# Kernel tuning notes

Measured on AMD Instinct MI355X. Metric: run time of the kernel, lower is better.

The kernel has to match this reference:

```python
import jax, jax.numpy as jnp
import numpy as np

H = 2048      # hidden_size
F = 768       # moe_intermediate_size
E = 32        # num_experts
K = 4         # num_experts_per_tok (top_k)
SF = 5632     # shared_expert_intermediate_size
B, S = 1, 2048


def setup_inputs() -> dict:
    key = jax.random.key(0)
    ks = jax.random.split(key, 9)
    rn = lambda k, sh, sc: (jax.random.normal(k, sh, jnp.float32) * sc)
    return {
        "hidden_states": rn(ks[0], (B, S, H), 1.0),
        "gate_w": rn(ks[1], (H, E), 0.02),                 # router Linear(H->E), no bias
        "wg": rn(ks[2], (E, H, F), H ** -0.5),             # expert gate_proj
        "wu": rn(ks[3], (E, H, F), H ** -0.5),             # expert up_proj
        "wd": rn(ks[4], (E, F, H), F ** -0.5),             # expert down_proj
        "sg": rn(ks[5], (H, SF), H ** -0.5),               # shared expert gate_proj
        "su": rn(ks[6], (H, SF), H ** -0.5),               # shared expert up_proj
        "sd": rn(ks[7], (SF, H), SF ** -0.5),              # shared expert down_proj
        "seg": rn(ks[8], (H, 1), H ** -0.5),               # shared_expert_gate Linear(H->1)
    }


def _moe_forward(x, gate_w, wg, wu, wd, sg, su, sd, seg):
    # x: [T, H] flattened tokens
    T = x.shape[0]
    logits = x @ gate_w                                    # [T, E]
    probs = jax.nn.softmax(logits, axis=-1)
    topw, topi = jax.lax.top_k(probs, K)                   # [T, K]
    topw = topw / jnp.sum(topw, axis=-1, keepdims=True)    # norm_topk_prob=True
    # dense combine weights [T, E] (expert ids per token are unique -> set is safe)
    combine = jnp.zeros((T, E), x.dtype).at[jnp.arange(T)[:, None], topi].set(topw)

    def body(acc, ew):
        wg_e, wu_e, wd_e, c_e = ew                         # [H,F],[H,F],[F,H],[T]
        h = jax.nn.silu(x @ wg_e) * (x @ wu_e)             # [T, F]
        return acc + c_e[:, None] * (h @ wd_e), None

    out, _ = jax.lax.scan(body, jnp.zeros_like(x), (wg, wu, wd, combine.T))

    shared = (jax.nn.silu(x @ sg) * (x @ su)) @ sd         # [T, H]
    out = out + jax.nn.sigmoid(x @ seg) * shared
    return out


def reference(hidden_states, gate_w, wg, wu, wd, sg, su, sd, seg):
    b, s, h = hidden_states.shape
    x = hidden_states.reshape(-1, h)
    out = _moe_forward(x, gate_w, wg, wu, wd, sg, su, sd, seg)
    return out.reshape(b, s, h)
```

## Files before the change

kernel.cpp:

```cpp
#include <hip/hip_runtime.h>
#include <hip/hip_bf16.h>
#include <math.h>

#define H_DIM 2048
#define F_DIM 768
#define E_NUM 32
#define TOPK 4
#define SF_DIM 5632
#define T_NUM 2048
#define P_MAX (T_NUM * TOPK)

typedef __attribute__((ext_vector_type(8))) short short8v;
typedef __attribute__((ext_vector_type(4))) float f4;
typedef unsigned short u16;

__device__ __forceinline__ u16 f2b(float f) {
  unsigned int u = __float_as_uint(f);
  u += 0x7FFFu + ((u >> 16) & 1u);
  return (u16)(u >> 16);
}

__device__ __forceinline__ f4 mfma16(short8v a, short8v b, f4 c) {
  return __builtin_amdgcn_mfma_f32_16x16x32_bf16(a, b, c, 0, 0, 0);
}

__device__ __forceinline__ void gld16(const u16* g, u16* l) {
  __builtin_amdgcn_global_load_lds(
      (const __attribute__((address_space(1))) void*)g,
      (__attribute__((address_space(3))) void*)l, 16, 0, 0);
}

__global__ __launch_bounds__(64) void router_kernel(
    const float* __restrict__ x, const float* __restrict__ gate_w,
    const float* __restrict__ seg, int* __restrict__ cnt,
    int* __restrict__ toklist, int* __restrict__ slotE,
    int* __restrict__ slotPos, float* __restrict__ wt4,
    float* __restrict__ sigbuf) {
  const int t = blockIdx.x;
  const int l = threadIdx.x;
  const int e = l & 31;
  const int half = l >> 5;
  const float* xr = x + (size_t)t * H_DIM;

  float acc = 0.0f, aseg = 0.0f;
  const int h0 = half * (H_DIM / 2);
  for (int h = 0; h < H_DIM / 2; ++h) {
    float xv = xr[h0 + h];
    acc += xv * gate_w[(h0 + h) * E_NUM + e];
    aseg += xv * seg[h0 + h];
  }
  acc += __shfl_xor(acc, 32, 64);
  aseg += __shfl_xor(aseg, 32, 64);

  float m = acc;
#pragma unroll
  for (int mask = 16; mask >= 1; mask >>= 1) m = fmaxf(m, __shfl_xor(m, mask, 64));
  float p = expf(acc - m);
  float s = p;
#pragma unroll
  for (int mask = 16; mask >= 1; mask >>= 1) s += __shfl_xor(s, mask, 64);
  p /= s;

  float pv = p;
  int ids[TOPK];
  float wv[TOPK];
  float wsum = 0.0f;
#pragma unroll
  for (int k = 0; k < TOPK; ++k) {
    float mv = pv;
    int mi = e;
#pragma unroll
    for (int mask = 16; mask >= 1; mask >>= 1) {
      float ov = __shfl_xor(mv, mask, 64);
      int oi = __shfl_xor(mi, mask, 64);
      if (ov > mv || (ov == mv && oi < mi)) { mv = ov; mi = oi; }
    }
    ids[k] = mi;
    wv[k] = mv;
    wsum += mv;
    if (e == mi) pv = -1.0f;
  }

  if (l < TOPK) {
    int id = ids[l];
    float w = wv[l] / wsum;
    int pos = atomicAdd(&cnt[id], 1);
    toklist[id * T_NUM + pos] = t;
    slotE[t * TOPK + l] = id;
    slotPos[t * TOPK + l] = pos;
    wt4[t * TOPK + l] = w;
  }
  if (l == 0) sigbuf[t] = 1.0f / (1.0f + expf(-aseg));
}

__global__ void offs_kernel(const int* __restrict__ cnt, int* __restrict__ offs) {
  if (threadIdx.x == 0) {
    int s = 0;
    for (int e = 0; e < E_NUM; ++e) { offs[e] = s; s += cnt[e]; }
  }
}

__global__ __launch_bounds__(256) void cvt_x(const float* __restrict__ in,
                                             u16* __restrict__ out) {
  int i = blockIdx.x * 256 + threadIdx.x;
  const float4* p = (const float4*)in + (size_t)i * 2;
  float4 a = p[0], b = p[1];
  short8v o;
  o[0] = (short)f2b(a.x); o[1] = (short)f2b(a.y);
  o[2] = (short)f2b(a.z); o[3] = (short)f2b(a.w);
  o[4] = (short)f2b(b.x); o[5] = (short)f2b(b.y);
  o[6] = (short)f2b(b.z); o[7] = (short)f2b(b.w);
  *(short8v*)(out + (size_t)i * 8) = o;
}

__global__ __launch_bounds__(256) void transpose_cvt(
    const float* __restrict__ in, u16* __restrict__ out, int R, int C) {
  in += (size_t)blockIdx.z * R * C;
  out += (size_t)blockIdx.z * R * C;
  const int r0 = blockIdx.y * 64;
  const int c0 = blockIdx.x * 64;
  __shared__ u16 tile[64][72];
  const int tid = threadIdx.x;
  const int tr = tid >> 2, tseg = tid & 3;
  const float* ip = in + (size_t)(r0 + tr) * C + c0 + tseg * 16;
#pragma unroll
  for (int j = 0; j < 4; ++j) {
    float4 v = *(const float4*)(ip + j * 4);
    u16* d = &tile[tr][tseg * 16 + j * 4];
    d[0] = f2b(v.x); d[1] = f2b(v.y); d[2] = f2b(v.z); d[3] = f2b(v.w);
  }
  __syncthreads();
  u16 tmp[16];
#pragma unroll
  for (int j = 0; j < 16; ++j) tmp[j] = tile[tseg * 16 + j][tr];
  u16* op = out + (size_t)(c0 + tr) * R + r0 + tseg * 16;
  *(short8v*)op = *(short8v*)&tmp[0];
  *(short8v*)(op + 8) = *(short8v*)&tmp[8];
}

__global__ __launch_bounds__(256) void gemm_gu(
    const u16* __restrict__ A, const u16* __restrict__ Bg,
    const u16* __restrict__ Bu, u16* __restrict__ Hout,
    int K, int N, int gather, const int* __restrict__ cnt,
    const int* __restrict__ toklist, const int* __restrict__ offs) {
  const int e = blockIdx.z;
  const int mtile = blockIdx.y;
  const int n0 = blockIdx.x * 64;
  int count = 1 << 30, obase = 0;
  if (gather) {
    count = cnt[e];
    if (mtile * 128 >= count) return;
    obase = offs[e];
    Bg += (size_t)e * N * K;
    Bu += (size_t)e * N * K;
  }

  __shared__ u16 As[128 * 32];
  __shared__ u16 Bgs[64 * 32];
  __shared__ u16 Bus[64 * 32];
  __shared__ int ids[128];

  const int tid = threadIdx.x;
  if (tid < 128) {
    int idx = mtile * 128 + tid;
    ids[tid] = gather ? toklist[e * T_NUM + min(idx, count - 1)] : idx;
  }
  __syncthreads();

  const int s = tid & 3, r0 = tid >> 2;
  const int cA0 = (s + (r0 >> 1)) & 3;
  const int cA1 = (s + ((r0 + 64) >> 1)) & 3;
  const u16* ap0 = A + (size_t)ids[r0] * K + cA0 * 8;
  const u16* ap1 = A + (size_t)ids[r0 + 64] * K + cA1 * 8;
  u16* al0 = As + tid * 8;
  u16* al1 = As + tid * 8 + 2048;
  const u16* bgp = Bg + (size_t)(n0 + r0) * K + cA0 * 8;
  const u16* bup = Bu + (size_t)(n0 + r0) * K + cA0 * 8;
  u16* bgl = Bgs + tid * 8;
  u16* bul = Bus + tid * 8;

  const int lane = tid & 63, w = tid >> 6;
  const int w0 = w & 1, w1 = w >> 1;
  const int ln = lane & 15, q = lane >> 4;

  int aoff[4], boff[2];
#pragma unroll
  for (int mt = 0; mt < 4; ++mt) {
    int r = w0 * 64 + mt * 16 + ln;
    aoff[mt] = r * 32 + ((q - (r >> 1)) & 3) * 8;
  }
#pragma unroll
  for (int nt = 0; nt < 2; ++nt) {
    int r = w1 * 32 + nt * 16 + ln;
    boff[nt] = r * 32 + ((q - (r >> 1)) & 3) * 8;
  }

  const f4 zero = {0.f, 0.f, 0.f, 0.f};
  f4 accg[4][2], accu[4][2];
#pragma unroll
  for (int mt = 0; mt < 4; ++mt)
#pragma unroll
    for (int nt = 0; nt < 2; ++nt) { accg[mt][nt] = zero; accu[mt][nt] = zero; }

  for (int k0 = 0; k0 < K; k0 += 32) {
    gld16(ap0 + k0, al0);
    gld16(ap1 + k0, al1);
    gld16(bgp + k0, bgl);
    gld16(bup + k0, bul);
    __syncthreads();
    short8v av[4], bgv[2], buv[2];
#pragma unroll
    for (int mt = 0; mt < 4; ++mt) av[mt] = *(const short8v*)&As[aoff[mt]];
#pragma unroll
    for (int nt = 0; nt < 2; ++nt) {
      bgv[nt] = *(const short8v*)&Bgs[boff[nt]];
      buv[nt] = *(const short8v*)&Bus[boff[nt]];
    }
#pragma unroll
    for (int mt = 0; mt < 4; ++mt)
#pragma unroll
      for (int nt = 0; nt < 2; ++nt) {
        accg[mt][nt] = mfma16(av[mt], bgv[nt], accg[mt][nt]);
        accu[mt][nt] = mfma16(av[mt], buv[nt], accu[mt][nt]);
      }
    __syncthreads();
  }

#pragma unroll
  for (int mt = 0; mt < 4; ++mt)
#pragma unroll
    for (int nt = 0; nt < 2; ++nt)
#pragma unroll
      for (int r = 0; r < 4; ++r) {
        int m = w0 * 64 + mt * 16 + 4 * q + r;
        int idx = mtile * 128 + m;
        if (idx < count) {
          int n = n0 + w1 * 32 + nt * 16 + ln;
          float g = accg[mt][nt][r], u = accu[mt][nt][r];
          float h = g / (1.0f + __expf(-g)) * u;
          Hout[(size_t)(obase + idx) * N + n] = f2b(h);
        }
      }
}

__global__ __launch_bounds__(256) void gemm_dn(
    const u16* __restrict__ A, const u16* __restrict__ Bt,
    float* __restrict__ D, int K, int N, int gather,
    const int* __restrict__ cnt, const int* __restrict__ offs) {
  const int e = blockIdx.z;
  const int mtile = blockIdx.y;
  const int n0 = blockIdx.x * 128;
  int count = 1 << 30, obase = 0;
  if (gather) {
    count = cnt[e];
    if (mtile * 128 >= count) return;
    obase = offs[e];
    Bt += (size_t)e * N * K;
  }

  __shared__ u16 As[128 * 32];
  __shared__ u16 Bs[128 * 32];
  __shared__ int ids[128];

  const int tid = threadIdx.x;
  if (tid < 128) {
    int idx = mtile * 128 + tid;
    ids[tid] = gather ? (obase + min(idx, count - 1)) : idx;
  }
  __syncthreads();

  const int s = tid & 3, r0 = tid >> 2;
  const int cA0 = (s + (r0 >> 1)) & 3;
  const int cA1 = (s + ((r0 + 64) >> 1)) & 3;
  const u16* ap0 = A + (size_t)ids[r0] * K + cA0 * 8;
  const u16* ap1 = A + (size_t)ids[r0 + 64] * K + cA1 * 8;
  u16* al0 = As + tid * 8;
  u16* al1 = As + tid * 8 + 2048;
  const u16* bp0 = Bt + (size_t)(n0 + r0) * K + cA0 * 8;
  const u16* bp1 = Bt + (size_t)(n0 + r0 + 64) * K + cA1 * 8;
  u16* bl0 = Bs + tid * 8;
  u16* bl1 = Bs + tid * 8 + 2048;

  const int lane = tid & 63, w = tid >> 6;
  const int w0 = w & 1, w1 = w >> 1;
  const int ln = lane & 15, q = lane >> 4;

  int aoff[4], boff[4];
#pragma unroll
  for (int mt = 0; mt < 4; ++mt) {
    int r = w0 * 64 + mt * 16 + ln;
    aoff[mt] = r * 32 + ((q - (r >> 1)) & 3) * 8;
    int rb = w1 * 64 + mt * 16 + ln;
    boff[mt] = rb * 32 + ((q - (rb >> 1)) & 3) * 8;
  }

  const f4 zero = {0.f, 0.f, 0.f, 0.f};
  f4 acc[4][4];
#pragma unroll
  for (int mt = 0; mt < 4; ++mt)
#pragma unroll
    for (int nt = 0; nt < 4; ++nt) acc[mt][nt] = zero;

  for (int k0 = 0; k0 < K; k0 += 32) {
    gld16(ap0 + k0, al0);
    gld16(ap1 + k0, al1);
    gld16(bp0 + k0, bl0);
    gld16(bp1 + k0, bl1);
    __syncthreads();
    short8v av[4], bv[4];
#pragma unroll
    for (int i = 0; i < 4; ++i) {
      av[i] = *(const short8v*)&As[aoff[i]];
      bv[i] = *(const short8v*)&Bs[boff[i]];
    }
#pragma unroll
    for (int mt = 0; mt < 4; ++mt)
#pragma unroll
      for (int nt = 0; nt < 4; ++nt)
        acc[mt][nt] = mfma16(av[mt], bv[nt], acc[mt][nt]);
    __syncthreads();
  }

#pragma unroll
  for (int mt = 0; mt < 4; ++mt)
#pragma unroll
    for (int nt = 0; nt < 4; ++nt)
#pragma unroll
      for (int r = 0; r < 4; ++r) {
        int m = w0 * 64 + mt * 16 + 4 * q + r;
        int idx = mtile * 128 + m;
        if (idx < count) {
          int n = n0 + w1 * 64 + nt * 16 + ln;
          D[(size_t)(obase + idx) * N + n] = acc[mt][nt][r];
        }
      }
}

__global__ __launch_bounds__(256) void combine_kernel(
    const float* __restrict__ sD, const float* __restrict__ Dh,
    const float* __restrict__ sig, const float* __restrict__ wt4,
    const int* __restrict__ slotE, const int* __restrict__ slotPos,
    const int* __restrict__ offs, float* __restrict__ out) {
  const int t = blockIdx.x;
  const int c = threadIdx.x * 8;
  const float sg = sig[t];
  const float* sp = sD + (size_t)t * H_DIM + c;
  float4 a0 = *(const float4*)sp;
  float4 a1 = *(const float4*)(sp + 4);
  float o[8];
  o[0] = sg * a0.x; o[1] = sg * a0.y; o[2] = sg * a0.z; o[3] = sg * a0.w;
  o[4] = sg * a1.x; o[5] = sg * a1.y; o[6] = sg * a1.z; o[7] = sg * a1.w;
#pragma unroll
  for (int k = 0; k < TOPK; ++k) {
    int ee = slotE[t * TOPK + k];
    int pp = offs[ee] + slotPos[t * TOPK + k];
    float w = wt4[t * TOPK + k];
    const float* dp = Dh + (size_t)pp * H_DIM + c;
    float4 d0 = *(const float4*)dp;
    float4 d1 = *(const float4*)(dp + 4);
    o[0] += w * d0.x; o[1] += w * d0.y; o[2] += w * d0.z; o[3] += w * d0.w;
    o[4] += w * d1.x; o[5] += w * d1.y; o[6] += w * d1.z; o[7] += w * d1.w;
  }
  float* op = out + (size_t)t * H_DIM + c;
  float4 r0 = {o[0], o[1], o[2], o[3]};
  float4 r1 = {o[4], o[5], o[6], o[7]};
  *(float4*)op = r0;
  *(float4*)(op + 4) = r1;
}

extern "C" void kernel_launch(void* const* d_in, const int* in_sizes, int n_in,
                              void* d_out, int out_size, void* d_ws, size_t ws_size,
                              hipStream_t stream) {
  const float* x      = (const float*)d_in[0];
  const float* gate_w = (const float*)d_in[1];
  const float* wg     = (const float*)d_in[2];
  const float* wu     = (const float*)d_in[3];
  const float* wd     = (const float*)d_in[4];
  const float* sg     = (const float*)d_in[5];
  const float* su     = (const float*)d_in[6];
  const float* sd     = (const float*)d_in[7];
  const float* seg    = (const float*)d_in[8];
  float* out = (float*)d_out;

  char* p = (char*)d_ws;
  auto alloc = [&](size_t bytes) {
    char* r = p;
    p += (bytes + 255) & ~(size_t)255;
    return r;
  };
  int* cnt      = (int*)alloc(E_NUM * 4);
  int* offs     = (int*)alloc(E_NUM * 4);
  int* toklist  = (int*)alloc((size_t)E_NUM * T_NUM * 4);
  int* slotE    = (int*)alloc((size_t)T_NUM * TOPK * 4);
  int* slotPos  = (int*)alloc((size_t)T_NUM * TOPK * 4);
  float* wt4    = (float*)alloc((size_t)T_NUM * TOPK * 4);
  float* sigbuf = (float*)alloc((size_t)T_NUM * 4);
  u16* xb  = (u16*)alloc((size_t)T_NUM * H_DIM * 2);
  u16* sgT = (u16*)alloc((size_t)H_DIM * SF_DIM * 2);
  u16* suT = (u16*)alloc((size_t)H_DIM * SF_DIM * 2);
  u16* sdT = (u16*)alloc((size_t)H_DIM * SF_DIM * 2);
  u16* wgT = (u16*)alloc((size_t)E_NUM * H_DIM * F_DIM * 2);
  u16* wuT = (u16*)alloc((size_t)E_NUM * H_DIM * F_DIM * 2);
  u16* wdT = (u16*)alloc((size_t)E_NUM * H_DIM * F_DIM * 2);
  u16* Hs  = (u16*)alloc((size_t)T_NUM * SF_DIM * 2);
  u16* He  = (u16*)alloc((size_t)(P_MAX + 128) * F_DIM * 2);
  float* sharedD = (float*)alloc((size_t)T_NUM * H_DIM * 4);
  float* Dh      = (float*)alloc((size_t)P_MAX * H_DIM * 4);

  hipMemsetAsync(cnt, 0, E_NUM * 4, stream);
  router_kernel<<<T_NUM, 64, 0, stream>>>(x, gate_w, seg, cnt, toklist,
                                          slotE, slotPos, wt4, sigbuf);
  offs_kernel<<<1, 64, 0, stream>>>(cnt, offs);

  cvt_x<<<(T_NUM * H_DIM / 8) / 256, 256, 0, stream>>>(x, xb);
  transpose_cvt<<<dim3(SF_DIM / 64, H_DIM / 64, 1), 256, 0, stream>>>(sg, sgT, H_DIM, SF_DIM);
  transpose_cvt<<<dim3(SF_DIM / 64, H_DIM / 64, 1), 256, 0, stream>>>(su, suT, H_DIM, SF_DIM);
  transpose_cvt<<<dim3(H_DIM / 64, SF_DIM / 64, 1), 256, 0, stream>>>(sd, sdT, SF_DIM, H_DIM);
  transpose_cvt<<<dim3(F_DIM / 64, H_DIM / 64, E_NUM), 256, 0, stream>>>(wg, wgT, H_DIM, F_DIM);
  transpose_cvt<<<dim3(F_DIM / 64, H_DIM / 64, E_NUM), 256, 0, stream>>>(wu, wuT, H_DIM, F_DIM);
  transpose_cvt<<<dim3(H_DIM / 64, F_DIM / 64, E_NUM), 256, 0, stream>>>(wd, wdT, F_DIM, H_DIM);

  gemm_gu<<<dim3(SF_DIM / 64, T_NUM / 128, 1), 256, 0, stream>>>(
      xb, sgT, suT, Hs, H_DIM, SF_DIM, 0, cnt, toklist, offs);
  gemm_gu<<<dim3(F_DIM / 64, T_NUM / 128, E_NUM), 256, 0, stream>>>(
      xb, wgT, wuT, He, H_DIM, F_DIM, 1, cnt, toklist, offs);
  gemm_dn<<<dim3(H_DIM / 128, T_NUM / 128, 1), 256, 0, stream>>>(
      Hs, sdT, sharedD, SF_DIM, H_DIM, 0, cnt, offs);
  gemm_dn<<<dim3(H_DIM / 128, T_NUM / 128, E_NUM), 256, 0, stream>>>(
      He, wdT, Dh, F_DIM, H_DIM, 1, cnt, offs);

  combine_kernel<<<T_NUM, 256, 0, stream>>>(sharedD, Dh, sigbuf, wt4,
                                            slotE, slotPos, offs, out);
}
```

Measured before the change: 1.313 ms.

## Merge shared and expert GEMMs into single launches and split-K the shared down-proj

Shared and routed-expert gate/up GEMMs now run in one flattened grid, and likewise the down-projection GEMMs, so the small shared-expert grids no longer leave the GPU underfilled between launches. The shared down-projection (K=5632, only 256 tiles) is split four ways along K into separate partial buffers, which the combine kernel sums before applying the sigmoid gate. This trades extra fp32 partial-output traffic and a larger buffer for more parallel work and fewer serialized launches.

Result: faster. 1.199 ms (-8.7%).

```diff
diff --git a/kernel.cpp b/kernel.cpp
--- a/kernel.cpp
+++ b/kernel.cpp
@@ -9,6 +9,12 @@
 #define SF_DIM 5632
 #define T_NUM 2048
 #define P_MAX (T_NUM * TOPK)
+#define KSPLIT 4
+
+#define NB_GU_SHARED ((SF_DIM / 64) * (T_NUM / 128))
+#define NB_GU_EXPERT ((F_DIM / 64) * (T_NUM / 128) * E_NUM)
+#define NB_DN_SHARED ((H_DIM / 128) * (T_NUM / 128) * KSPLIT)
+#define NB_DN_EXPERT ((H_DIM / 128) * (T_NUM / 128) * E_NUM)
 
 typedef __attribute__((ext_vector_type(8))) short short8v;
 typedef __attribute__((ext_vector_type(4))) float f4;
@@ -138,21 +144,34 @@
   *(short8v*)(op + 8) = *(short8v*)&tmp[8];
 }
 
-__global__ __launch_bounds__(256) void gemm_gu(
-    const u16* __restrict__ A, const u16* __restrict__ Bg,
-    const u16* __restrict__ Bu, u16* __restrict__ Hout,
-    int K, int N, int gather, const int* __restrict__ cnt,
+__global__ __launch_bounds__(256) void gemm_gu_all(
+    const u16* __restrict__ A, const u16* __restrict__ sgT,
+    const u16* __restrict__ suT, u16* __restrict__ HsOut,
+    const u16* __restrict__ wgT, const u16* __restrict__ wuT,
+    u16* __restrict__ HeOut, const int* __restrict__ cnt,
     const int* __restrict__ toklist, const int* __restrict__ offs) {
-  const int e = blockIdx.z;
-  const int mtile = blockIdx.y;
-  const int n0 = blockIdx.x * 64;
-  int count = 1 << 30, obase = 0;
-  if (gather) {
+  const int bid = blockIdx.x;
+  const int K = H_DIM;
+  const u16 *Bg, *Bu;
+  u16* Hout;
+  int n0, mtile, count, obase, N, gather, e = 0;
+  if (bid < NB_GU_SHARED) {
+    mtile = bid / (SF_DIM / 64);
+    n0 = (bid % (SF_DIM / 64)) * 64;
+    count = 1 << 30; obase = 0; N = SF_DIM; gather = 0;
+    Bg = sgT; Bu = suT; Hout = HsOut;
+  } else {
+    const int r = bid - NB_GU_SHARED;
+    e = r / ((F_DIM / 64) * (T_NUM / 128));
+    const int rem = r % ((F_DIM / 64) * (T_NUM / 128));
+    mtile = rem / (F_DIM / 64);
+    n0 = (rem % (F_DIM / 64)) * 64;
     count = cnt[e];
     if (mtile * 128 >= count) return;
-    obase = offs[e];
-    Bg += (size_t)e * N * K;
-    Bu += (size_t)e * N * K;
+    obase = offs[e]; N = F_DIM; gather = 1;
+    Bg = wgT + (size_t)e * F_DIM * H_DIM;
+    Bu = wuT + (size_t)e * F_DIM * H_DIM;
+    Hout = HeOut;
   }
 
   __shared__ u16 As[128 * 32];
@@ -243,19 +262,36 @@
       }
 }
 
-__global__ __launch_bounds__(256) void gemm_dn(
-    const u16* __restrict__ A, const u16* __restrict__ Bt,
-    float* __restrict__ D, int K, int N, int gather,
+__global__ __launch_bounds__(256) void gemm_dn_all(
+    const u16* __restrict__ HsIn, const u16* __restrict__ sdT,
+    float* __restrict__ sharedD, const u16* __restrict__ HeIn,
+    const u16* __restrict__ wdT, float* __restrict__ Dh,
     const int* __restrict__ cnt, const int* __restrict__ offs) {
-  const int e = blockIdx.z;
-  const int mtile = blockIdx.y;
-  const int n0 = blockIdx.x * 128;
-  int count = 1 << 30, obase = 0;
-  if (gather) {
+  const int bid = blockIdx.x;
+  const u16 *Ap, *Bt;
+  float* D;
+  int n0, mtile, count, obase, K, kbeg, klen, gather;
+  if (bid < NB_DN_SHARED) {
+    const int kz = bid / ((H_DIM / 128) * (T_NUM / 128));
+    const int rem = bid % ((H_DIM / 128) * (T_NUM / 128));
+    mtile = rem / (H_DIM / 128);
+    n0 = (rem % (H_DIM / 128)) * 128;
+    count = 1 << 30; obase = 0; gather = 0;
+    K = SF_DIM; klen = SF_DIM / KSPLIT; kbeg = kz * klen;
+    Ap = HsIn; Bt = sdT;
+    D = sharedD + (size_t)kz * T_NUM * H_DIM;
+  } else {
+    const int r = bid - NB_DN_SHARED;
+    const int e = r / ((H_DIM / 128) * (T_NUM / 128));
+    const int rem = r % ((H_DIM / 128) * (T_NUM / 128));
+    mtile = rem / (H_DIM / 128);
+    n0 = (rem % (H_DIM / 128)) * 128;
     count = cnt[e];
     if (mtile * 128 >= count) return;
-    obase = offs[e];
-    Bt += (size_t)e * N * K;
+    obase = offs[e]; gather = 1;
+    K = F_DIM; klen = F_DIM; kbeg = 0;
+    Ap = HeIn; Bt = wdT + (size_t)e * H_DIM * F_DIM;
+    D = Dh;
   }
 
   __shared__ u16 As[128 * 32];
@@ -272,12 +308,12 @@
   const int s = tid & 3, r0 = tid >> 2;
   const int cA0 = (s + (r0 >> 1)) & 3;
   const int cA1 = (s + ((r0 + 64) >> 1)) & 3;
-  const u16* ap0 = A + (size_t)ids[r0] * K + cA0 * 8;
-  const u16* ap1 = A + (size_t)ids[r0 + 64] * K + cA1 * 8;
+  const u16* ap0 = Ap + (size_t)ids[r0] * K + kbeg + cA0 * 8;
+  const u16* ap1 = Ap + (size_t)ids[r0 + 64] * K + kbeg + cA1 * 8;
   u16* al0 = As + tid * 8;
   u16* al1 = As + tid * 8 + 2048;
-  const u16* bp0 = Bt + (size_t)(n0 + r0) * K + cA0 * 8;
-  const u16* bp1 = Bt + (size_t)(n0 + r0 + 64) * K + cA1 * 8;
+  const u16* bp0 = Bt + (size_t)(n0 + r0) * K + kbeg + cA0 * 8;
+  const u16* bp1 = Bt + (size_t)(n0 + r0 + 64) * K + kbeg + cA1 * 8;
   u16* bl0 = Bs + tid * 8;
   u16* bl1 = Bs + tid * 8 + 2048;
 
@@ -301,7 +337,7 @@
 #pragma unroll
     for (int nt = 0; nt < 4; ++nt) acc[mt][nt] = zero;
 
-  for (int k0 = 0; k0 < K; k0 += 32) {
+  for (int k0 = 0; k0 < klen; k0 += 32) {
     gld16(ap0 + k0, al0);
     gld16(ap1 + k0, al1);
     gld16(bp0 + k0, bl0);
@@ -331,7 +367,7 @@
         int idx = mtile * 128 + m;
         if (idx < count) {
           int n = n0 + w1 * 64 + nt * 16 + ln;
-          D[(size_t)(obase + idx) * N + n] = acc[mt][nt][r];
+          D[(size_t)(obase + idx) * H_DIM + n] = acc[mt][nt][r];
         }
       }
 }
@@ -344,12 +380,17 @@
   const int t = blockIdx.x;
   const int c = threadIdx.x * 8;
   const float sg = sig[t];
-  const float* sp = sD + (size_t)t * H_DIM + c;
-  float4 a0 = *(const float4*)sp;
-  float4 a1 = *(const float4*)(sp + 4);
-  float o[8];
-  o[0] = sg * a0.x; o[1] = sg * a0.y; o[2] = sg * a0.z; o[3] = sg * a0.w;
-  o[4] = sg * a1.x; o[5] = sg * a1.y; o[6] = sg * a1.z; o[7] = sg * a1.w;
+  float o[8] = {0.f, 0.f, 0.f, 0.f, 0.f, 0.f, 0.f, 0.f};
+#pragma unroll
+  for (int z = 0; z < KSPLIT; ++z) {
+    const float* sp = sD + ((size_t)z * T_NUM + t) * H_DIM + c;
+    float4 a0 = *(const float4*)sp;
+    float4 a1 = *(const float4*)(sp + 4);
+    o[0] += a0.x; o[1] += a0.y; o[2] += a0.z; o[3] += a0.w;
+    o[4] += a1.x; o[5] += a1.y; o[6] += a1.z; o[7] += a1.w;
+  }
+#pragma unroll
+  for (int j = 0; j < 8; ++j) o[j] *= sg;
 #pragma unroll
   for (int k = 0; k < TOPK; ++k) {
     int ee = slotE[t * TOPK + k];
@@ -404,7 +445,7 @@
   u16* wdT = (u16*)alloc((size_t)E_NUM * H_DIM * F_DIM * 2);
   u16* Hs  = (u16*)alloc((size_t)T_NUM * SF_DIM * 2);
   u16* He  = (u16*)alloc((size_t)(P_MAX + 128) * F_DIM * 2);
-  float* sharedD = (float*)alloc((size_t)T_NUM * H_DIM * 4);
+  float* sharedD = (float*)alloc((size_t)KSPLIT * T_NUM * H_DIM * 4);
   float* Dh      = (float*)alloc((size_t)P_MAX * H_DIM * 4);
 
   hipMemsetAsync(cnt, 0, E_NUM * 4, stream);
@@ -420,14 +461,10 @@
   transpose_cvt<<<dim3(F_DIM / 64, H_DIM / 64, E_NUM), 256, 0, stream>>>(wu, wuT, H_DIM, F_DIM);
   transpose_cvt<<<dim3(H_DIM / 64, F_DIM / 64, E_NUM), 256, 0, stream>>>(wd, wdT, F_DIM, H_DIM);
 
-  gemm_gu<<<dim3(SF_DIM / 64, T_NUM / 128, 1), 256, 0, stream>>>(
-      xb, sgT, suT, Hs, H_DIM, SF_DIM, 0, cnt, toklist, offs);
-  gemm_gu<<<dim3(F_DIM / 64, T_NUM / 128, E_NUM), 256, 0, stream>>>(
-      xb, wgT, wuT, He, H_DIM, F_DIM, 1, cnt, toklist, offs);
-  gemm_dn<<<dim3(H_DIM / 128, T_NUM / 128, 1), 256, 0, stream>>>(
-      Hs, sdT, sharedD, SF_DIM, H_DIM, 0, cnt, offs);
-  gemm_dn<<<dim3(H_DIM / 128, T_NUM / 128, E_NUM), 256, 0, stream>>>(
-      He, wdT, Dh, F_DIM, H_DIM, 1, cnt, offs);
+  gemm_gu_all<<<NB_GU_SHARED + NB_GU_EXPERT, 256, 0, stream>>>(
+      xb, sgT, suT, Hs, wgT, wuT, He, cnt, toklist, offs);
+  gemm_dn_all<<<NB_DN_SHARED + NB_DN_EXPERT, 256, 0, stream>>>(
+      Hs, sdT, sharedD, He, wdT, Dh, cnt, offs);
 
   combine_kernel<<<T_NUM, 256, 0, stream>>>(sharedD, Dh, sigbuf, wt4,
                                             slotE, slotPos, offs, out);
```
